# Kernel optimization log

Measured on AMD Instinct MI355X. Metric: run time of the kernel, lower is better.

The kernel has to match this reference:

```python
import jax, jax.numpy as jnp
import numpy as np

IN_CAPS = 32
IN_CH = 8
OUT_CAPS = 10
OUT_CH = 16
NUM_ROUTING = 3
WID = 6
HEI = 6
BATCH = 64


def setup_inputs() -> dict:
    key = jax.random.key(0)
    k1, k2 = jax.random.split(key)
    u = jax.random.normal(k1, (BATCH, IN_CAPS, IN_CH, WID, HEI), dtype=jnp.float32)
    W = jax.random.normal(k2, (IN_CAPS, IN_CH, WID, HEI, OUT_CAPS, OUT_CH), dtype=jnp.float32) * 0.05
    return {"u": u, "W": W}


def reference(u, W):
    # u: [B, ic, ich, w, h]; W: [ic, ich, w, h, oc, och]
    B = u.shape[0]
    # _mul_1: broadcast multiply then fold (ich*w*h) into one axis
    u_hat = (u[..., None, None] * W[None]).reshape(
        B, IN_CAPS, IN_CH * WID * HEI, OUT_CAPS, OUT_CH
    )  # [B, ic, D, oc, och]
    u_sum = u_hat.sum(axis=2)            # [B, ic, oc, och] (used every iteration in _mul_2)
    u_dot = u_hat.sum(axis=(0, 2, 4))    # [ic, oc] (constant part of _dot)
    b_ij = jnp.zeros((IN_CAPS, OUT_CAPS), dtype=u.dtype)
    v_j = None
    for _ in range(NUM_ROUTING):
        c_ij = jax.nn.softmax(b_ij, axis=0)                     # softmax over in_capsules
        s_j = jnp.einsum('io,bioc->boc', c_ij, u_sum)           # [B, oc, och]
        # squash with GLOBAL L1 norm (torch .norm(1) over all elements) -- faithful to source
        n = jnp.abs(s_j).sum()
        v_j = (n * n) / (1.0 + n * n) * (s_j / n)               # [B, oc, och]
        agree = u_dot * v_j.sum(axis=(0, 2))[None, :]           # [ic, oc]
        b_ij = b_ij + jax.lax.stop_gradient(agree)              # torch uses .data (detached)
    return v_j
```

## Files before the change

kernel.cpp:

```cpp
#include <hip/hip_runtime.h>
#include <math.h>

#define B_   64
#define IC   32
#define D_   288
#define OC   10
#define OCH  16
#define J_   160
#define BJ   10240
#define POISON 0xAAAAAAAAu

__global__ __launch_bounds__(320) void k_usum(const float* __restrict__ u,
                                              const float* __restrict__ Wt,
                                              float* __restrict__ US,
                                              float* __restrict__ UDp) {
    const int ic  = blockIdx.x & 31;
    const int bt  = blockIdx.x >> 5;
    const int tid = threadIdx.x;
    __shared__ float u_lds[4 * D_];
    __shared__ float part[640];
    __shared__ float ud_part[OC];
    if (tid < OC) ud_part[tid] = 0.f;
    for (int idx = tid; idx < 288; idx += 320) {
        int b_sub = idx / 72;
        int f4    = idx - b_sub * 72;
        int b     = bt * 4 + b_sub;
        ((float4*)u_lds)[idx] =
            ((const float4*)(u + (size_t)(b * IC + ic) * D_))[f4];
    }
    __syncthreads();
    const int j4    = tid % 40;
    const int b_sub = (tid / 40) & 3;
    const int dh    = tid / 160;
    const float4* wp = (const float4*)(Wt + (size_t)ic * D_ * J_)
                       + (size_t)dh * 144 * 40 + j4;
    const float*  ur = u_lds + b_sub * D_ + dh * 144;
    float ax = 0.f, ay = 0.f, az = 0.f, aw = 0.f;
    for (int d0 = 0; d0 < 144; d0 += 16) {
        float4 w[16];
        #pragma unroll
        for (int k = 0; k < 16; ++k) w[k] = wp[(d0 + k) * 40];
        #pragma unroll
        for (int k = 0; k < 16; ++k) {
            float uv = ur[d0 + k];
            ax += uv * w[k].x; ay += uv * w[k].y;
            az += uv * w[k].z; aw += uv * w[k].w;
        }
    }
    if (dh == 1) ((float4*)part)[tid - 160] = make_float4(ax, ay, az, aw);
    __syncthreads();
    if (dh == 0) {
        float4 p = ((float4*)part)[tid];
        ax += p.x; ay += p.y; az += p.z; aw += p.w;
        ((float4*)(US + (size_t)ic * BJ + (bt * 4 + b_sub) * J_))[j4] =
            make_float4(ax, ay, az, aw);
        float g = ax + ay + az + aw;
        g += __shfl_xor(g, 1);
        g += __shfl_xor(g, 2);
        if ((tid & 3) == 0) atomicAdd(&ud_part[j4 >> 2], g);
    }
    __syncthreads();
    if (tid < OC) UDp[blockIdx.x * OC + tid] = ud_part[tid];
}

__global__ __launch_bounds__(320) void k_route(const float* __restrict__ US,
                                               const float* __restrict__ UDp,
                                               unsigned* __restrict__ npart,
                                               unsigned* __restrict__ nres,
                                               float* __restrict__ out) {
    const int bid = blockIdx.x;
    const int tid = threadIdx.x;
    const int i   = tid & 31;
    const int o   = tid >> 5;
    __shared__ float cij[OC * IC];
    __shared__ float wred[5];
    __shared__ float nsh;
    const int t  = bid * 320 + tid;
    const int ot = (t >> 4) % OC;
    float us[IC];
    #pragma unroll
    for (int ii = 0; ii < IC; ++ii) us[ii] = US[(size_t)ii * BJ + t];
    float udv = 0.f;
    #pragma unroll
    for (int bt = 0; bt < 16; ++bt) udv += UDp[(bt * 32 + i) * OC + o];
    float bij = 0.f;
    for (int q = 0; q < 3; ++q) {
        float m = bij;
        m = fmaxf(m, __shfl_xor(m, 16, 32));
        m = fmaxf(m, __shfl_xor(m,  8, 32));
        m = fmaxf(m, __shfl_xor(m,  4, 32));
        m = fmaxf(m, __shfl_xor(m,  2, 32));
        m = fmaxf(m, __shfl_xor(m,  1, 32));
        float e  = __expf(bij - m);
        float se = e;
        se += __shfl_xor(se, 16, 32);
        se += __shfl_xor(se,  8, 32);
        se += __shfl_xor(se,  4, 32);
        se += __shfl_xor(se,  2, 32);
        se += __shfl_xor(se,  1, 32);
        float c = e / se;
        cij[o * IC + i] = c;
        float cs = c * udv;
        cs += __shfl_xor(cs, 16, 32);
        cs += __shfl_xor(cs,  8, 32);
        cs += __shfl_xor(cs,  4, 32);
        cs += __shfl_xor(cs,  2, 32);
        cs += __shfl_xor(cs,  1, 32);
        __syncthreads();
        float s = 0.f;
        {
            const float* cp = cij + ot * IC;
            #pragma unroll
            for (int ii = 0; ii < IC; ++ii) s += cp[ii] * us[ii];
        }
        float a = fabsf(s);
        #pragma unroll
        for (int off = 32; off; off >>= 1) a += __shfl_down(a, off);
        if ((tid & 63) == 0) wred[tid >> 6] = a;
        __syncthreads();
        if (tid == 0)
            __hip_atomic_store(&npart[q * 32 + bid],
                               __float_as_uint(wred[0] + wred[1] + wred[2] +
                                               wred[3] + wred[4]),
                               __ATOMIC_RELEASE, __HIP_MEMORY_SCOPE_AGENT);
        if (bid == 0 && tid < 32) {
            unsigned v;
            do {
                v = __hip_atomic_load(&npart[q * 32 + tid], __ATOMIC_ACQUIRE,
                                      __HIP_MEMORY_SCOPE_AGENT);
            } while (v == POISON);
            float p = __uint_as_float(v);
            p += __shfl_xor(p, 16, 32);
            p += __shfl_xor(p,  8, 32);
            p += __shfl_xor(p,  4, 32);
            p += __shfl_xor(p,  2, 32);
            p += __shfl_xor(p,  1, 32);
            if (tid == 0)
                __hip_atomic_store(&nres[q], __float_as_uint(p),
                                   __ATOMIC_RELEASE, __HIP_MEMORY_SCOPE_AGENT);
        }
        if (tid == 0) {
            unsigned v;
            while ((v = __hip_atomic_load(&nres[q], __ATOMIC_ACQUIRE,
                                          __HIP_MEMORY_SCOPE_AGENT)) == POISON)
                __builtin_amdgcn_s_sleep(1);
            nsh = __uint_as_float(v);
        }
        __syncthreads();
        const float n  = nsh;
        const float n2 = n * n;
        if (q < 2) {
            bij += udv * ((n2 / (1.f + n2)) * (cs / n));
        } else {
            out[t] = (n2 / (1.f + n2)) * (s / n);
        }
        __syncthreads();
    }
}

extern "C" void kernel_launch(void* const* d_in, const int* in_sizes, int n_in,
                              void* d_out, int out_size, void* d_ws, size_t ws_size,
                              hipStream_t stream) {
    (void)in_sizes; (void)n_in; (void)out_size; (void)ws_size;
    const float* u  = (const float*)d_in[0];
    const float* Wt = (const float*)d_in[1];
    float* ws      = (float*)d_ws;
    float*    US    = ws;
    float*    UDp   = ws + 327680;
    unsigned* npart = (unsigned*)(ws + 332800);
    unsigned* nres  = (unsigned*)(ws + 332928);

    k_usum<<<dim3(512), dim3(320), 0, stream>>>(u, Wt, US, UDp);
    k_route<<<dim3(32), dim3(320), 0, stream>>>(US, UDp, npart, nres,
                                                (float*)d_out);
}
```

Before: 82.05 us.

## Fuse u_sum and routing kernels into one launch with grid-wide flag barrier

Merges the two kernels into a single launch. Each of the 512 blocks publishes a completion flag after writing its US/UDp slice, and the first 32 blocks spin on all flags before running the routing iterations. Spin-loop atomics are relaxed to relaxed ordering, with a single acquire load after the wait. This removes the second kernel launch and the inter-kernel gap, but it relies on blocks 0-31 being co-resident with the others and on the relaxed-then-acquire pattern being enough for memory visibility.

```diff
diff --git a/kernel.cpp b/kernel.cpp
--- a/kernel.cpp
+++ b/kernel.cpp
@@ -10,16 +10,24 @@
 #define BJ   10240
 #define POISON 0xAAAAAAAAu
 
-__global__ __launch_bounds__(320) void k_usum(const float* __restrict__ u,
+__global__ __launch_bounds__(320) void k_caps(const float* __restrict__ u,
                                               const float* __restrict__ Wt,
                                               float* __restrict__ US,
-                                              float* __restrict__ UDp) {
-    const int ic  = blockIdx.x & 31;
-    const int bt  = blockIdx.x >> 5;
+                                              float* __restrict__ UDp,
+                                              unsigned* __restrict__ flag1,
+                                              unsigned* __restrict__ npart,
+                                              unsigned* __restrict__ nres,
+                                              float* __restrict__ out) {
+    const int bid = blockIdx.x;
+    const int ic  = bid & 31;
+    const int bt  = bid >> 5;
     const int tid = threadIdx.x;
     __shared__ float u_lds[4 * D_];
     __shared__ float part[640];
     __shared__ float ud_part[OC];
+    __shared__ float cij[OC * IC];
+    __shared__ float wred[5];
+    __shared__ float nsh;
     if (tid < OC) ud_part[tid] = 0.f;
     for (int idx = tid; idx < 288; idx += 320) {
         int b_sub = idx / 72;
@@ -60,21 +68,24 @@
         if ((tid & 3) == 0) atomicAdd(&ud_part[j4 >> 2], g);
     }
     __syncthreads();
-    if (tid < OC) UDp[blockIdx.x * OC + tid] = ud_part[tid];
-}
+    if (tid < OC) UDp[bid * OC + tid] = ud_part[tid];
+    __syncthreads();
+    if (tid == 0)
+        __hip_atomic_store(&flag1[bid], 1u, __ATOMIC_RELEASE,
+                           __HIP_MEMORY_SCOPE_AGENT);
+    if (bid >= 32) return;
 
-__global__ __launch_bounds__(320) void k_route(const float* __restrict__ US,
-                                               const float* __restrict__ UDp,
-                                               unsigned* __restrict__ npart,
-                                               unsigned* __restrict__ nres,
-                                               float* __restrict__ out) {
-    const int bid = blockIdx.x;
-    const int tid = threadIdx.x;
-    const int i   = tid & 31;
-    const int o   = tid >> 5;
-    __shared__ float cij[OC * IC];
-    __shared__ float wred[5];
-    __shared__ float nsh;
+    for (int f = tid; f < 512; f += 320)
+        while (__hip_atomic_load(&flag1[f], __ATOMIC_RELAXED,
+                                 __HIP_MEMORY_SCOPE_AGENT) == POISON)
+            __builtin_amdgcn_s_sleep(1);
+    __syncthreads();
+    if (tid == 0)
+        (void)__hip_atomic_load(&flag1[0], __ATOMIC_ACQUIRE,
+                                __HIP_MEMORY_SCOPE_AGENT);
+    __syncthreads();
+    const int i  = tid & 31;
+    const int o  = tid >> 5;
     const int t  = bid * 320 + tid;
     const int ot = (t >> 4) % OC;
     float us[IC];
@@ -82,7 +93,7 @@
     for (int ii = 0; ii < IC; ++ii) us[ii] = US[(size_t)ii * BJ + t];
     float udv = 0.f;
     #pragma unroll
-    for (int bt = 0; bt < 16; ++bt) udv += UDp[(bt * 32 + i) * OC + o];
+    for (int btt = 0; btt < 16; ++btt) udv += UDp[(btt * 32 + i) * OC + o];
     float bij = 0.f;
     for (int q = 0; q < 3; ++q) {
         float m = bij;
@@ -126,7 +137,7 @@
         if (bid == 0 && tid < 32) {
             unsigned v;
             do {
-                v = __hip_atomic_load(&npart[q * 32 + tid], __ATOMIC_ACQUIRE,
+                v = __hip_atomic_load(&npart[q * 32 + tid], __ATOMIC_RELAXED,
                                       __HIP_MEMORY_SCOPE_AGENT);
             } while (v == POISON);
             float p = __uint_as_float(v);
@@ -141,7 +152,7 @@
         }
         if (tid == 0) {
             unsigned v;
-            while ((v = __hip_atomic_load(&nres[q], __ATOMIC_ACQUIRE,
+            while ((v = __hip_atomic_load(&nres[q], __ATOMIC_RELAXED,
                                           __HIP_MEMORY_SCOPE_AGENT)) == POISON)
                 __builtin_amdgcn_s_sleep(1);
             nsh = __uint_as_float(v);
@@ -164,13 +175,13 @@
     (void)in_sizes; (void)n_in; (void)out_size; (void)ws_size;
     const float* u  = (const float*)d_in[0];
     const float* Wt = (const float*)d_in[1];
-    float* ws      = (float*)d_ws;
+    float* ws = (float*)d_ws;
     float*    US    = ws;
     float*    UDp   = ws + 327680;
-    unsigned* npart = (unsigned*)(ws + 332800);
-    unsigned* nres  = (unsigned*)(ws + 332928);
+    unsigned* flag1 = (unsigned*)(ws + 332800);
+    unsigned* npart = (unsigned*)(ws + 333312);
+    unsigned* nres  = (unsigned*)(ws + 333440);
 
-    k_usum<<<dim3(512), dim3(320), 0, stream>>>(u, Wt, US, UDp);
-    k_route<<<dim3(32), dim3(320), 0, stream>>>(US, UDp, npart, nres,
-                                                (float*)d_out);
+    k_caps<<<dim3(512), dim3(320), 0, stream>>>(u, Wt, US, UDp, flag1, npart,
+                                                nres, (float*)d_out);
 }
```

Result: slower. 94.13 us (+14.7%).

## Stage W tiles in LDS with double buffering and widen batch tile to 8

Applied to the files above, without the earlier changes.

The u_sum kernel now has each block handle 8 batch rows instead of 4, halving the grid to 256 blocks. W chunks of 24 rows are staged into a double-buffered LDS array shared by all 8 batch rows, with the next chunk prefetched into registers during compute, replacing the direct global W reads and the split-D partial reduction. This halves total W global traffic but lowers parallelism and adds a barrier per chunk. The routing kernel's spin loads are relaxed to plain atomic loads and the UDp partial count is adjusted to 8.

```diff
diff --git a/kernel.cpp b/kernel.cpp
--- a/kernel.cpp
+++ b/kernel.cpp
@@ -17,48 +17,56 @@
     const int ic  = blockIdx.x & 31;
     const int bt  = blockIdx.x >> 5;
     const int tid = threadIdx.x;
-    __shared__ float u_lds[4 * D_];
-    __shared__ float part[640];
-    __shared__ float ud_part[OC];
+    __shared__ float  u_lds[8 * D_];
+    __shared__ float4 wbuf[2][960];
+    __shared__ float  ud_part[OC];
     if (tid < OC) ud_part[tid] = 0.f;
-    for (int idx = tid; idx < 288; idx += 320) {
-        int b_sub = idx / 72;
-        int f4    = idx - b_sub * 72;
-        int b     = bt * 4 + b_sub;
-        ((float4*)u_lds)[idx] =
-            ((const float4*)(u + (size_t)(b * IC + ic) * D_))[f4];
+    #pragma unroll
+    for (int k = 0; k < 2; ++k) {
+        int idx = tid + k * 320;
+        if (idx < 576) {
+            int b_sub = idx / 72, f4 = idx - b_sub * 72;
+            int b = bt * 8 + b_sub;
+            ((float4*)u_lds)[idx] =
+                ((const float4*)u)[(size_t)(b * IC + ic) * (D_ / 4) + f4];
+        }
     }
+    const float4* wg = (const float4*)(Wt + (size_t)ic * D_ * J_);
+    #pragma unroll
+    for (int k = 0; k < 3; ++k)
+        wbuf[0][tid + k * 320] = wg[tid + k * 320];
     __syncthreads();
     const int j4    = tid % 40;
-    const int b_sub = (tid / 40) & 3;
-    const int dh    = tid / 160;
-    const float4* wp = (const float4*)(Wt + (size_t)ic * D_ * J_)
-                       + (size_t)dh * 144 * 40 + j4;
-    const float*  ur = u_lds + b_sub * D_ + dh * 144;
+    const int b_sub = tid / 40;
     float ax = 0.f, ay = 0.f, az = 0.f, aw = 0.f;
-    for (int d0 = 0; d0 < 144; d0 += 16) {
-        float4 w[16];
+    for (int c = 0; c < 12; ++c) {
+        const int cur = c & 1;
+        float4 wn[3];
+        if (c < 11) {
+            #pragma unroll
+            for (int k = 0; k < 3; ++k)
+                wn[k] = wg[(c + 1) * 960 + tid + k * 320];
+        }
+        const float* uc = u_lds + b_sub * D_ + c * 24;
         #pragma unroll
-        for (int k = 0; k < 16; ++k) w[k] = wp[(d0 + k) * 40];
-        #pragma unroll
-        for (int k = 0; k < 16; ++k) {
-            float uv = ur[d0 + k];
-            ax += uv * w[k].x; ay += uv * w[k].y;
-            az += uv * w[k].z; aw += uv * w[k].w;
+        for (int dl = 0; dl < 24; ++dl) {
+            float4 w  = wbuf[cur][dl * 40 + j4];
+            float  uv = uc[dl];
+            ax += uv * w.x; ay += uv * w.y; az += uv * w.z; aw += uv * w.w;
         }
+        if (c < 11) {
+            #pragma unroll
+            for (int k = 0; k < 3; ++k)
+                wbuf[cur ^ 1][tid + k * 320] = wn[k];
+        }
+        __syncthreads();
     }
-    if (dh == 1) ((float4*)part)[tid - 160] = make_float4(ax, ay, az, aw);
-    __syncthreads();
-    if (dh == 0) {
-        float4 p = ((float4*)part)[tid];
-        ax += p.x; ay += p.y; az += p.z; aw += p.w;
-        ((float4*)(US + (size_t)ic * BJ + (bt * 4 + b_sub) * J_))[j4] =
-            make_float4(ax, ay, az, aw);
-        float g = ax + ay + az + aw;
-        g += __shfl_xor(g, 1);
-        g += __shfl_xor(g, 2);
-        if ((tid & 3) == 0) atomicAdd(&ud_part[j4 >> 2], g);
-    }
+    ((float4*)(US + (size_t)ic * BJ + (bt * 8 + b_sub) * J_))[j4] =
+        make_float4(ax, ay, az, aw);
+    float g = ax + ay + az + aw;
+    g += __shfl_xor(g, 1);
+    g += __shfl_xor(g, 2);
+    if ((tid & 3) == 0) atomicAdd(&ud_part[j4 >> 2], g);
     __syncthreads();
     if (tid < OC) UDp[blockIdx.x * OC + tid] = ud_part[tid];
 }
@@ -82,7 +90,7 @@
     for (int ii = 0; ii < IC; ++ii) us[ii] = US[(size_t)ii * BJ + t];
     float udv = 0.f;
     #pragma unroll
-    for (int bt = 0; bt < 16; ++bt) udv += UDp[(bt * 32 + i) * OC + o];
+    for (int bt = 0; bt < 8; ++bt) udv += UDp[(bt * 32 + i) * OC + o];
     float bij = 0.f;
     for (int q = 0; q < 3; ++q) {
         float m = bij;
@@ -126,7 +134,7 @@
         if (bid == 0 && tid < 32) {
             unsigned v;
             do {
-                v = __hip_atomic_load(&npart[q * 32 + tid], __ATOMIC_ACQUIRE,
+                v = __hip_atomic_load(&npart[q * 32 + tid], __ATOMIC_RELAXED,
                                       __HIP_MEMORY_SCOPE_AGENT);
             } while (v == POISON);
             float p = __uint_as_float(v);
@@ -141,7 +149,7 @@
         }
         if (tid == 0) {
             unsigned v;
-            while ((v = __hip_atomic_load(&nres[q], __ATOMIC_ACQUIRE,
+            while ((v = __hip_atomic_load(&nres[q], __ATOMIC_RELAXED,
                                           __HIP_MEMORY_SCOPE_AGENT)) == POISON)
                 __builtin_amdgcn_s_sleep(1);
             nsh = __uint_as_float(v);
@@ -164,13 +172,13 @@
     (void)in_sizes; (void)n_in; (void)out_size; (void)ws_size;
     const float* u  = (const float*)d_in[0];
     const float* Wt = (const float*)d_in[1];
-    float* ws      = (float*)d_ws;
+    float* ws = (float*)d_ws;
     float*    US    = ws;
     float*    UDp   = ws + 327680;
-    unsigned* npart = (unsigned*)(ws + 332800);
-    unsigned* nres  = (unsigned*)(ws + 332928);
+    unsigned* npart = (unsigned*)(ws + 330240);
+    unsigned* nres  = (unsigned*)(ws + 330368);
 
-    k_usum<<<dim3(512), dim3(320), 0, stream>>>(u, Wt, US, UDp);
+    k_usum<<<dim3(256), dim3(320), 0, stream>>>(u, Wt, US, UDp);
     k_route<<<dim3(32), dim3(320), 0, stream>>>(US, UDp, npart, nres,
                                                 (float*)d_out);
 }
```

Result: slower. 85.56 us (+4.3%).
